# Kernel tuning notes

Hardware: AMD Instinct MI355X
Metric: run time of the kernel (lower is better)

The kernel has to match this reference:

```python
import jax, jax.numpy as jnp
import numpy as np

WIN = 7
SHIFT = 3
HEADS = 6
EPS = 1e-5


def _rel_pos_index(ws):
    coords = np.stack(np.meshgrid(np.arange(ws), np.arange(ws), indexing='ij')).reshape(2, -1)
    rel = (coords[:, :, None] - coords[:, None, :]).transpose(1, 2, 0)  # (N, N, 2)
    rel[..., 0] += ws - 1
    rel[..., 1] += ws - 1
    rel[..., 0] *= 2 * ws - 1
    return jnp.asarray(rel.sum(-1).reshape(-1))  # (N*N,)


def _attn_mask(H, W, ws, ss):
    img = np.zeros((H, W))
    sl = (slice(0, -ws), slice(-ws, -ss), slice(-ss, None))
    cnt = 0
    for hs in sl:
        for wss in sl:
            img[hs, wss] = cnt
            cnt += 1
    mw = img.reshape(H // ws, ws, W // ws, ws).transpose(0, 2, 1, 3).reshape(-1, ws * ws)
    am = mw[:, None, :] - mw[:, :, None]  # (nw, N, N): mw[j]-mw[i]
    return jnp.asarray(np.where(am != 0, -1e9, 0.0).astype(np.float32))


def _layernorm(x, g, b):
    mu = x.mean(-1, keepdims=True)
    var = ((x - mu) ** 2).mean(-1, keepdims=True)
    return (x - mu) * jax.lax.rsqrt(var + EPS) * g + b


def setup_inputs() -> dict:
    key = jax.random.key(0)
    ks = jax.random.split(key, 6)
    B, H, W, C = 4, 224, 224, 192
    return {
        'x': jax.random.normal(ks[0], (B, H * W, C), jnp.float32),
        'norm1_g': jnp.ones((C,), jnp.float32),
        'norm1_b': jnp.zeros((C,), jnp.float32),
        'qkv_w': jax.random.normal(ks[1], (C, 3 * C), jnp.float32) * 0.02,
        'qkv_b': jnp.zeros((3 * C,), jnp.float32),
        'rpb_table': jax.random.normal(ks[2], ((2 * WIN - 1) ** 2, HEADS), jnp.float32) * 0.02,
        'proj_w': jax.random.normal(ks[3], (C, C), jnp.float32) * 0.02,
        'proj_b': jnp.zeros((C,), jnp.float32),
        'norm2_g': jnp.ones((C,), jnp.float32),
        'norm2_b': jnp.zeros((C,), jnp.float32),
        'fc1_w': jax.random.normal(ks[4], (C, 4 * C), jnp.float32) * 0.02,
        'fc1_b': jnp.zeros((4 * C,), jnp.float32),
        'fc2_w': jax.random.normal(ks[5], (4 * C, C), jnp.float32) * 0.02,
        'fc2_b': jnp.zeros((C,), jnp.float32),
        'h': 224,
        'w': 224,
    }


def reference(x, norm1_g, norm1_b, qkv_w, qkv_b, rpb_table, proj_w, proj_b,
              norm2_g, norm2_b, fc1_w, fc1_b, fc2_w, fc2_b, h, w):
    B, L, C = x.shape
    ch = C // HEADS
    N = WIN * WIN
    nh, nw = h // WIN, w // WIN
    rel_idx = _rel_pos_index(WIN)
    mask = _attn_mask(h, w, WIN, SHIFT)  # (nh*nw, N, N)

    shortcut = x
    xn = _layernorm(x, norm1_g, norm1_b).reshape(B, h, w, C)
    xs = jnp.roll(xn, (-SHIFT, -SHIFT), axis=(1, 2))
    # window partition -> (B*nh*nw, N, C)
    xw = xs.reshape(B, nh, WIN, nw, WIN, C).transpose(0, 1, 3, 2, 4, 5).reshape(B * nh * nw, N, C)

    qkv = (xw @ qkv_w + qkv_b).reshape(-1, N, 3, HEADS, ch).transpose(2, 0, 3, 1, 4)
    q, k, v = qkv[0], qkv[1], qkv[2]  # (NW, HEADS, N, ch)
    scale = ch ** -0.5
    attn = jnp.einsum('whic,whjc->whij', q * scale, k)
    bias = rpb_table[rel_idx].reshape(N, N, HEADS).transpose(2, 0, 1)  # (HEADS, N, N)
    attn = attn + bias[None]
    attn = attn.reshape(B, nh * nw, HEADS, N, N) + mask[None, :, None]
    attn = jax.nn.softmax(attn, axis=-1).reshape(B * nh * nw, HEADS, N, N)

    out = jnp.einsum('whij,whjc->whic', attn, v).transpose(0, 2, 1, 3).reshape(-1, N, C)
    out = out @ proj_w + proj_b
    # window reverse + roll back
    out = out.reshape(B, nh, nw, WIN, WIN, C).transpose(0, 1, 3, 2, 4, 5).reshape(B, h, w, C)
    out = jnp.roll(out, (SHIFT, SHIFT), axis=(1, 2)).reshape(B, L, C)

    x = shortcut + out
    xn2 = _layernorm(x, norm2_g, norm2_b)
    hid = jax.nn.gelu(xn2 @ fc1_w + fc1_b, approximate=False)
    return x + (hid @ fc2_w + fc2_b)
```

## Files before the change

kernel.cpp:

```cpp
#include <hip/hip_runtime.h>
#include <stdint.h>

#define MB    50176
#define CDIM  192

typedef __attribute__((ext_vector_type(8))) short bf16x8;
typedef __attribute__((ext_vector_type(4))) float f32x4;

__device__ __forceinline__ float wsum(float v){
  #pragma unroll
  for (int m=32;m>=1;m>>=1) v += __shfl_xor(v,m,64);
  return v;
}
__device__ __forceinline__ float bfbits2f(uint32_t h){
  union{uint32_t u; float f;} x; x.u = h<<16; return x.f;
}
__device__ __forceinline__ uint16_t f2bfbits(float f){
  union{float ff; uint32_t u;} x; x.ff = f;
  return (uint16_t)((x.u + 0x7FFFu + ((x.u>>16)&1u)) >> 16);
}
__device__ __forceinline__ void gload16(const void* g, void* l){
  __builtin_amdgcn_global_load_lds(
      (const __attribute__((address_space(1))) uint32_t*)g,
      (__attribute__((address_space(3))) uint32_t*)l, 16, 0, 0);
}
__device__ __forceinline__ size_t row2tok(int r_g){
  int widx = r_g/49, tpos = r_g - widx*49;
  int b = widx>>10, rem = widx&1023;
  int h = (rem>>5)*7 + tpos/7 + 3; if (h>=224) h-=224;
  int w = (rem&31)*7 + (tpos - (tpos/7)*7) + 3; if (w>=224) w-=224;
  return (size_t)b*MB + (size_t)h*224 + w;
}

__global__ __launch_bounds__(256) void prep_kernel(
    const float* __restrict__ qkv_w, const float* __restrict__ proj_w,
    const float* __restrict__ fc1_w, const float* __restrict__ fc2_w,
    const float* __restrict__ rpb,
    uint16_t* __restrict__ qkvW, uint16_t* __restrict__ prjW,
    uint16_t* __restrict__ fc1W, uint16_t* __restrict__ fc2W,
    float* __restrict__ btbl){
  int idx = blockIdx.x*256 + threadIdx.x;
  if (idx < 110592){ int k=idx/576, n=idx-k*576; qkvW[n*192+k]=f2bfbits(qkv_w[idx]); return; }
  idx -= 110592;
  if (idx < 36864){ int k=idx/192, n=idx-k*192; prjW[n*192+k]=f2bfbits(proj_w[idx]); return; }
  idx -= 36864;
  if (idx < 147456){ int k=idx/768, n=idx-k*768; fc1W[n*192+k]=f2bfbits(fc1_w[idx]); return; }
  idx -= 147456;
  if (idx < 147456){ int k=idx/192, n=idx-k*192; fc2W[n*768+k]=f2bfbits(fc2_w[idx]); return; }
  idx -= 147456;
  if (idx >= 98304) return;
  int j = idx & 63, i = (idx>>6) & 63;
  int hd = (idx>>12) % 6, cls = (idx>>12)/6;
  float v = -1e9f;
  if (i < 49 && j < 49){
    int dh = i/7 - j/7, dw = i%7 - j%7;
    v = rpb[((dh+6)*13 + (dw+6))*6 + hd];
    int cH = cls>>1, cW = cls&1;
    int li = (cH ? (i/7 < 4 ? 1 : 2) : 0)*3 + (cW ? (i%7 < 4 ? 1 : 2) : 0);
    int lj = (cH ? (j/7 < 4 ? 1 : 2) : 0)*3 + (cW ? (j%7 < 4 ? 1 : 2) : 0);
    if (li != lj) v = -1e9f;
  }
  btbl[idx] = v;
}

__global__ __launch_bounds__(256) void ln1_kernel(
    const float* __restrict__ x, const float* __restrict__ g,
    const float* __restrict__ bt, uint16_t* __restrict__ dst, int row0){
  int wid_l = (int)((blockIdx.x*256u + threadIdx.x) >> 6);
  int lane  = threadIdx.x & 63;
  size_t sidx = row2tok(row0 + wid_l);
  const float* s = x + sidx*CDIM;
  float v0=s[lane], v1=s[lane+64], v2=s[lane+128];
  float mu  = wsum(v0+v1+v2) * (1.f/192.f);
  float var = wsum(v0*v0+v1*v1+v2*v2)*(1.f/192.f) - mu*mu;
  float rs  = rsqrtf(var + 1e-5f);
  uint16_t* d = dst + (size_t)wid_l*CDIM;
  d[lane]     = f2bfbits((v0-mu)*rs*g[lane]     + bt[lane]);
  d[lane+64]  = f2bfbits((v1-mu)*rs*g[lane+64]  + bt[lane+64]);
  d[lane+128] = f2bfbits((v2-mu)*rs*g[lane+128] + bt[lane+128]);
}

enum { EPI_QKV=0, EPI_FC1=2, EPI_FC2=3 };

template<int EPI, int K, int NN>
__global__ __launch_bounds__(256) void mgemm(
    const uint16_t* __restrict__ A, const uint16_t* __restrict__ WT,
    const float* __restrict__ bias, void* __restrict__ outp,
    const float* __restrict__ resid, int row0){
  __shared__ __attribute__((aligned(16))) char As[128*128];
  __shared__ __attribute__((aligned(16))) char Bs[64*128];
  const int tid  = threadIdx.x;
  const int lane = tid & 63;
  const int wid  = tid >> 6;
  const int brow = blockIdx.y * 128;
  const int bcol = blockIdx.x * 64;

  f32x4 acc[4][2];
  #pragma unroll
  for (int m=0;m<4;m++)
    #pragma unroll
    for (int n=0;n<2;n++) acc[m][n] = (f32x4){0.f,0.f,0.f,0.f};

  const int srow = lane >> 3;
  const int sg   = (lane & 7) ^ srow;
  const int wm = wid >> 1, wn = wid & 1;
  const int lrow16 = lane & 15, lkh = lane >> 4;

  for (int k0 = 0; k0 < K; k0 += 64){
    #pragma unroll
    for (int c = 0; c < 4; c++){
      int ch = wid*4 + c;
      gload16(A + (size_t)(brow + ch*8 + srow)*K + k0 + sg*8, As + ch*1024);
    }
    #pragma unroll
    for (int c = 0; c < 2; c++){
      int ch = wid*2 + c;
      gload16(WT + (size_t)(bcol + ch*8 + srow)*K + k0 + sg*8, Bs + ch*1024);
    }
    __syncthreads();

    bf16x8 af[4][2], bfr[2][2];
    #pragma unroll
    for (int m=0;m<4;m++)
      #pragma unroll
      for (int ks=0;ks<2;ks++){
        int arow = wm*64 + m*16 + lrow16;
        af[m][ks] = *(const bf16x8*)(As + arow*128 + (((ks*4+lkh) ^ (arow&7))<<4));
      }
    #pragma unroll
    for (int n=0;n<2;n++)
      #pragma unroll
      for (int ks=0;ks<2;ks++){
        int brn = wn*32 + n*16 + lrow16;
        bfr[n][ks] = *(const bf16x8*)(Bs + brn*128 + (((ks*4+lkh) ^ (brn&7))<<4));
      }
    #pragma unroll
    for (int m=0;m<4;m++)
      #pragma unroll
      for (int n=0;n<2;n++)
        #pragma unroll
        for (int ks=0;ks<2;ks++)
          acc[m][n] = __builtin_amdgcn_mfma_f32_16x16x32_bf16(
              af[m][ks], bfr[n][ks], acc[m][n], 0, 0, 0);
    __syncthreads();
  }

  float bi[2];
  #pragma unroll
  for (int n=0;n<2;n++) bi[n] = bias[bcol + wn*32 + n*16 + lrow16];
  #pragma unroll
  for (int m=0;m<4;m++){
    #pragma unroll
    for (int j=0;j<4;j++){
      int r = brow + wm*64 + m*16 + lkh*4 + j;
      if constexpr (EPI==EPI_QKV || EPI==EPI_FC1){
        #pragma unroll
        for (int n=0;n<2;n++){
          float v = acc[m][n][j] + bi[n];
          if constexpr (EPI==EPI_FC1)
            v = 0.5f*v*(1.f + erff(v*0.70710678118654752f));
          ((uint16_t*)outp)[(size_t)r*NN + bcol + wn*32 + n*16 + lrow16] = f2bfbits(v);
        }
      } else {
        size_t pr = row2tok(row0 + r)*CDIM;
        #pragma unroll
        for (int n=0;n<2;n++){
          size_t p = pr + bcol + wn*32 + n*16 + lrow16;
          ((float*)outp)[p] = acc[m][n][j] + bi[n] + resid[p];
        }
      }
    }
  }
}

__global__ __launch_bounds__(384) void proj_ln2(
    const uint16_t* __restrict__ A, const uint16_t* __restrict__ WT,
    const float* __restrict__ pbias, const float* __restrict__ x,
    const float* __restrict__ g2, const float* __restrict__ b2,
    float* __restrict__ xout, uint16_t* __restrict__ ln2out, int row0){
  __shared__ __attribute__((aligned(16))) char As[128*128];
  __shared__ __attribute__((aligned(16))) char Bs[192*128];
  __shared__ float stats[3][128][2];
  const int tid  = threadIdx.x;
  const int lane = tid & 63;
  const int wid  = tid >> 6;
  const int wm = wid >> 2, wn3 = wid & 3;
  const int pm = wid / 3, pn = wid - pm*3;
  const int brow = blockIdx.x * 128;
  const int srow = lane >> 3;
  const int sg   = (lane & 7) ^ srow;
  const int lrow16 = lane & 15, lkh = lane >> 4;
  (void)wm; (void)wn3;

  f32x4 acc[4][4];
  #pragma unroll
  for (int m=0;m<4;m++)
    #pragma unroll
    for (int n=0;n<4;n++) acc[m][n] = (f32x4){0.f,0.f,0.f,0.f};

  for (int k0 = 0; k0 < 192; k0 += 64){
    for (int ch = wid; ch < 16; ch += 6)
      gload16(A + (size_t)(brow + ch*8 + srow)*192 + k0 + sg*8, As + ch*1024);
    for (int ch = wid; ch < 24; ch += 6)
      gload16(WT + (size_t)(ch*8 + srow)*192 + k0 + sg*8, Bs + ch*1024);
    __syncthreads();

    bf16x8 af[4][2], bfr[4][2];
    #pragma unroll
    for (int m=0;m<4;m++)
      #pragma unroll
      for (int ks=0;ks<2;ks++){
        int arow = pm*64 + m*16 + lrow16;
        af[m][ks] = *(const bf16x8*)(As + arow*128 + (((ks*4+lkh) ^ (arow&7))<<4));
      }
    #pragma unroll
    for (int n=0;n<4;n++)
      #pragma unroll
      for (int ks=0;ks<2;ks++){
        int brn = pn*64 + n*16 + lrow16;
        bfr[n][ks] = *(const bf16x8*)(Bs + brn*128 + (((ks*4+lkh) ^ (brn&7))<<4));
      }
    #pragma unroll
    for (int m=0;m<4;m++)
      #pragma unroll
      for (int n=0;n<4;n++)
        #pragma unroll
        for (int ks=0;ks<2;ks++)
          acc[m][n] = __builtin_amdgcn_mfma_f32_16x16x32_bf16(
              af[m][ks], bfr[n][ks], acc[m][n], 0, 0, 0);
    __syncthreads();
  }

  float bi[4], g2v[4], b2v[4];
  #pragma unroll
  for (int n=0;n<4;n++){
    int c = pn*64 + n*16 + lrow16;
    bi[n] = pbias[c]; g2v[n] = g2[c]; b2v[n] = b2[c];
  }
  #pragma unroll
  for (int m=0;m<4;m++){
    #pragma unroll
    for (int j=0;j<4;j++){
      int r = pm*64 + m*16 + lkh*4 + j;
      size_t pr = row2tok(row0 + brow + r)*CDIM;
      float s1 = 0.f, s2 = 0.f;
      #pragma unroll
      for (int n=0;n<4;n++){
        int c = pn*64 + n*16 + lrow16;
        float y = acc[m][n][j] + bi[n] + x[pr + c];
        acc[m][n][j] = y;
        xout[pr + c] = y;
        s1 += y; s2 = fmaf(y, y, s2);
      }
      #pragma unroll
      for (int mk=1; mk<16; mk<<=1){
        s1 += __shfl_xor(s1, mk, 64);
        s2 += __shfl_xor(s2, mk, 64);
      }
      if (lrow16 == 0){ stats[pn][r][0] = s1; stats[pn][r][1] = s2; }
    }
  }
  __syncthreads();
  #pragma unroll
  for (int m=0;m<4;m++){
    #pragma unroll
    for (int j=0;j<4;j++){
      int r = pm*64 + m*16 + lkh*4 + j;
      float s1 = stats[0][r][0] + stats[1][r][0] + stats[2][r][0];
      float s2 = stats[0][r][1] + stats[1][r][1] + stats[2][r][1];
      float mu = s1*(1.f/192.f);
      float rs = rsqrtf(s2*(1.f/192.f) - mu*mu + 1e-5f);
      size_t pr = (size_t)(brow + r)*CDIM;
      #pragma unroll
      for (int n=0;n<4;n++){
        int c = pn*64 + n*16 + lrow16;
        ln2out[pr + c] = f2bfbits((acc[m][n][j]-mu)*rs*g2v[n] + b2v[n]);
      }
    }
  }
}

__global__ __launch_bounds__(64) void attn_kernel(
    const uint16_t* __restrict__ qkv, const float* __restrict__ btbl,
    uint16_t* __restrict__ attnout, int win0){
  const int bid  = blockIdx.x;
  const int widx = bid/6, hd = bid - widx*6;
  const int lane = threadIdx.x;
  const int r16 = lane & 15, t4 = lane >> 4;
  __shared__ uint16_t Vt[32][72];
  __shared__ uint16_t Pl[16][72];

  #pragma unroll
  for (int e=lane; e<32*16; e+=64){ Vt[e>>4][48 + (e&15)] = 0; }
  for (int ch = lane; ch < 196; ch += 64){
    int j = ch >> 2, c0 = (ch&3)*8;
    const uint16_t* src = qkv + ((size_t)widx*49 + j)*576 + hd*32 + 384 + c0;
    uint4 v = *(const uint4*)src;
    uint32_t u[4] = {v.x, v.y, v.z, v.w};
    #pragma unroll
    for (int q=0;q<8;q++) Vt[c0+q][j] = (uint16_t)(u[q>>1] >> ((q&1)*16));
  }

  bf16x8 kf[4], qf[4];
  #pragma unroll
  for (int jt=0;jt<4;jt++)
    kf[jt] = *(const bf16x8*)(qkv + ((size_t)widx*49 + jt*16 + r16)*576 + hd*32 + 192 + t4*8);
  #pragma unroll
  for (int it=0;it<4;it++)
    qf[it] = *(const bf16x8*)(qkv + ((size_t)widx*49 + it*16 + r16)*576 + hd*32 + t4*8);
  f32x4 acc[4][4];
  #pragma unroll
  for (int jt=0;jt<4;jt++)
    #pragma unroll
    for (int it=0;it<4;it++){
      acc[jt][it] = (f32x4){0.f,0.f,0.f,0.f};
      acc[jt][it] = __builtin_amdgcn_mfma_f32_16x16x32_bf16(kf[jt], qf[it], acc[jt][it], 0,0,0);
    }
  __syncthreads();

  const int gw = win0 + widx;
  const int cls = ((((gw&1023)>>5)==31)<<1) | ((gw&31)==31);
  const float* tb = btbl + ((size_t)(cls*6 + hd) << 12);
  const float scale = 0.17677669529663689f;

  bf16x8 bv[2][2];
  #pragma unroll
  for (int ct=0;ct<2;ct++)
    #pragma unroll
    for (int ks=0;ks<2;ks++)
      bv[ct][ks] = *(const bf16x8*)&Vt[ct*16 + r16][ks*32 + t4*8];

  #pragma unroll
  for (int it=0;it<4;it++){
    int i = it*16 + r16;
    float s[4][4];
    float m = -3.4e38f;
    #pragma unroll
    for (int jt=0;jt<4;jt++){
      float4 bvv = *(const float4*)(tb + i*64 + jt*16 + t4*4);
      float bb[4] = {bvv.x, bvv.y, bvv.z, bvv.w};
      #pragma unroll
      for (int r=0;r<4;r++){
        s[jt][r] = acc[jt][it][r]*scale + bb[r];
        m = fmaxf(m, s[jt][r]);
      }
    }
    m = fmaxf(m, __shfl_xor(m, 16, 64));
    m = fmaxf(m, __shfl_xor(m, 32, 64));
    float sum = 0.f;
    #pragma unroll
    for (int jt=0;jt<4;jt++)
      #pragma unroll
      for (int r=0;r<4;r++){
        s[jt][r] = __expf(s[jt][r] - m);
        sum += s[jt][r];
      }
    sum += __shfl_xor(sum, 16, 64);
    sum += __shfl_xor(sum, 32, 64);
    float inv = 1.f / sum;
    #pragma unroll
    for (int jt=0;jt<4;jt++){
      uint32_t lo = (uint32_t)f2bfbits(s[jt][0]*inv) | ((uint32_t)f2bfbits(s[jt][1]*inv) << 16);
      uint32_t hi = (uint32_t)f2bfbits(s[jt][2]*inv) | ((uint32_t)f2bfbits(s[jt][3]*inv) << 16);
      *(uint2*)&Pl[r16][jt*16 + t4*4] = make_uint2(lo, hi);
    }
    __syncthreads();

    f32x4 o[2];
    o[0] = (f32x4){0.f,0.f,0.f,0.f};
    o[1] = (f32x4){0.f,0.f,0.f,0.f};
    #pragma unroll
    for (int ks=0;ks<2;ks++){
      bf16x8 pa = *(const bf16x8*)&Pl[r16][ks*32 + t4*8];
      #pragma unroll
      for (int ct=0;ct<2;ct++)
        o[ct] = __builtin_amdgcn_mfma_f32_16x16x32_bf16(pa, bv[ct][ks], o[ct], 0,0,0);
    }
    #pragma unroll
    for (int r=0;r<4;r++){
      int i2 = it*16 + t4*4 + r;
      if (i2 < 49){
        size_t base = ((size_t)widx*49 + i2)*CDIM + hd*32;
        attnout[base + r16]      = f2bfbits(o[0][r]);
        attnout[base + 16 + r16] = f2bfbits(o[1][r]);
      }
    }
  }
}

extern "C" void kernel_launch(void* const* d_in, const int* in_sizes, int n_in,
                              void* d_out, int out_size, void* d_ws, size_t ws_size,
                              hipStream_t stream) {
  const float* x       = (const float*)d_in[0];
  const float* n1g     = (const float*)d_in[1];
  const float* n1b     = (const float*)d_in[2];
  const float* qkv_w   = (const float*)d_in[3];
  const float* qkv_b   = (const float*)d_in[4];
  const float* rpb     = (const float*)d_in[5];
  const float* proj_w  = (const float*)d_in[6];
  const float* proj_b  = (const float*)d_in[7];
  const float* n2g     = (const float*)d_in[8];
  const float* n2b     = (const float*)d_in[9];
  const float* fc1_w   = (const float*)d_in[10];
  const float* fc1_b   = (const float*)d_in[11];
  const float* fc2_w   = (const float*)d_in[12];
  const float* fc2_b   = (const float*)d_in[13];
  float* out = (float*)d_out;

  const size_t TBL = 221184 + 73728 + 294912 + 294912 + 393216;
  size_t need_full = (size_t)200704*CDIM*2 + (size_t)200704*768*2 + TBL;
  bool full = ws_size >= need_full;
  int T  = full ? 200704 : MB;
  int NC = full ? 1 : 4;
  int NW = T / 49;

  char* ws = (char*)d_ws;
  uint16_t* Abuf = (uint16_t*)ws;
  uint16_t* Bq   = (uint16_t*)(ws + (size_t)T*CDIM*2);
  char* wbase    = ws + (size_t)T*CDIM*2 + (size_t)T*768*2;
  uint16_t* qkvW = (uint16_t*)wbase;
  uint16_t* prjW = (uint16_t*)(wbase + 221184);
  uint16_t* fc1W = (uint16_t*)(wbase + 221184 + 73728);
  uint16_t* fc2W = (uint16_t*)(wbase + 221184 + 73728 + 294912);
  float*    btbl = (float*)(wbase + 221184 + 73728 + 294912 + 294912);

  prep_kernel<<<2112, 256, 0, stream>>>(qkv_w, proj_w, fc1_w, fc2_w, rpb,
                                        qkvW, prjW, fc1W, fc2W, btbl);

  for (int c = 0; c < NC; c++){
    int row0 = c*T, win0 = row0/49;
    ln1_kernel<<<T/4, 256, 0, stream>>>(x, n1g, n1b, Abuf, row0);
    mgemm<EPI_QKV, 192, 576>
        <<<dim3(9, T/128), 256, 0, stream>>>(Abuf, qkvW, qkv_b, (void*)Bq, nullptr, 0);
    attn_kernel<<<NW*6, 64, 0, stream>>>(Bq, btbl, Abuf, win0);
    proj_ln2<<<T/128, 384, 0, stream>>>(Abuf, prjW, proj_b, x, n2g, n2b,
                                        out, Abuf, row0);
    mgemm<EPI_FC1, 192, 768>
        <<<dim3(12, T/128), 256, 0, stream>>>(Abuf, fc1W, fc1_b, (void*)Bq, nullptr, 0);
    mgemm<EPI_FC2, 768, 192>
        <<<dim3(3, T/128), 256, 0, stream>>>(Bq, fc2W, fc2_b, (void*)out, out, row0);
  }
}
```

Baseline: 798.3 us.

## Fuse FC1+GELU and FC2 into one MLP kernel keeping hidden chunks in LDS

Replaces the separate FC1 (with GELU, writing a bf16 hidden tensor of width 768) and FC2 GEMM launches with a single kernel. Each 64-row block computes the hidden activations in chunks of 96, keeps them in shared memory and accumulates the FC2 output in registers, then adds bias and residual. This removes the global round trip of the large hidden tensor and lets the workspace shrink. In exchange, weights are read straight from global memory per block with no LDS staging, and fc1 weights are re-streamed for every 64-row block.

```diff
diff --git a/kernel.cpp b/kernel.cpp
--- a/kernel.cpp
+++ b/kernel.cpp
@@ -80,13 +80,9 @@
   d[lane+128] = f2bfbits((v2-mu)*rs*g[lane+128] + bt[lane+128]);
 }
 
-enum { EPI_QKV=0, EPI_FC1=2, EPI_FC2=3 };
-
-template<int EPI, int K, int NN>
-__global__ __launch_bounds__(256) void mgemm(
+__global__ __launch_bounds__(256) void qkv_gemm(
     const uint16_t* __restrict__ A, const uint16_t* __restrict__ WT,
-    const float* __restrict__ bias, void* __restrict__ outp,
-    const float* __restrict__ resid, int row0){
+    const float* __restrict__ bias, uint16_t* __restrict__ outp){
   __shared__ __attribute__((aligned(16))) char As[128*128];
   __shared__ __attribute__((aligned(16))) char Bs[64*128];
   const int tid  = threadIdx.x;
@@ -106,16 +102,16 @@
   const int wm = wid >> 1, wn = wid & 1;
   const int lrow16 = lane & 15, lkh = lane >> 4;
 
-  for (int k0 = 0; k0 < K; k0 += 64){
+  for (int k0 = 0; k0 < 192; k0 += 64){
     #pragma unroll
     for (int c = 0; c < 4; c++){
       int ch = wid*4 + c;
-      gload16(A + (size_t)(brow + ch*8 + srow)*K + k0 + sg*8, As + ch*1024);
+      gload16(A + (size_t)(brow + ch*8 + srow)*192 + k0 + sg*8, As + ch*1024);
     }
     #pragma unroll
     for (int c = 0; c < 2; c++){
       int ch = wid*2 + c;
-      gload16(WT + (size_t)(bcol + ch*8 + srow)*K + k0 + sg*8, Bs + ch*1024);
+      gload16(WT + (size_t)(bcol + ch*8 + srow)*192 + k0 + sg*8, Bs + ch*1024);
     }
     __syncthreads();
 
@@ -153,21 +149,10 @@
     #pragma unroll
     for (int j=0;j<4;j++){
       int r = brow + wm*64 + m*16 + lkh*4 + j;
-      if constexpr (EPI==EPI_QKV || EPI==EPI_FC1){
-        #pragma unroll
-        for (int n=0;n<2;n++){
-          float v = acc[m][n][j] + bi[n];
-          if constexpr (EPI==EPI_FC1)
-            v = 0.5f*v*(1.f + erff(v*0.70710678118654752f));
-          ((uint16_t*)outp)[(size_t)r*NN + bcol + wn*32 + n*16 + lrow16] = f2bfbits(v);
-        }
-      } else {
-        size_t pr = row2tok(row0 + r)*CDIM;
-        #pragma unroll
-        for (int n=0;n<2;n++){
-          size_t p = pr + bcol + wn*32 + n*16 + lrow16;
-          ((float*)outp)[p] = acc[m][n][j] + bi[n] + resid[p];
-        }
+      #pragma unroll
+      for (int n=0;n<2;n++){
+        float v = acc[m][n][j] + bi[n];
+        outp[(size_t)r*576 + bcol + wn*32 + n*16 + lrow16] = f2bfbits(v);
       }
     }
   }
@@ -184,13 +169,11 @@
   const int tid  = threadIdx.x;
   const int lane = tid & 63;
   const int wid  = tid >> 6;
-  const int wm = wid >> 2, wn3 = wid & 3;
   const int pm = wid / 3, pn = wid - pm*3;
   const int brow = blockIdx.x * 128;
   const int srow = lane >> 3;
   const int sg   = (lane & 7) ^ srow;
   const int lrow16 = lane & 15, lkh = lane >> 4;
-  (void)wm; (void)wn3;
 
   f32x4 acc[4][4];
   #pragma unroll
@@ -275,6 +258,101 @@
       for (int n=0;n<4;n++){
         int c = pn*64 + n*16 + lrow16;
         ln2out[pr + c] = f2bfbits((acc[m][n][j]-mu)*rs*g2v[n] + b2v[n]);
+      }
+    }
+  }
+}
+
+__global__ __launch_bounds__(384) void mlp_kernel(
+    const uint16_t* __restrict__ A,
+    const uint16_t* __restrict__ W1T,
+    const uint16_t* __restrict__ W2T,
+    const float* __restrict__ b1, const float* __restrict__ b2,
+    const float* __restrict__ resid,
+    float* __restrict__ out, int row0){
+  __shared__ uint16_t hidc[64][104];
+  const int tid  = threadIdx.x;
+  const int lane = tid & 63, wid = tid >> 6;
+  const int pm = wid / 3, pn = wid - pm*3;
+  const int r16 = lane & 15, t4 = lane >> 4;
+  const int brow = blockIdx.x * 64;
+
+  bf16x8 af[2][6];
+  #pragma unroll
+  for (int m=0;m<2;m++)
+    #pragma unroll
+    for (int ks=0;ks<6;ks++)
+      af[m][ks] = *(const bf16x8*)(A + (size_t)(brow + pm*32 + m*16 + r16)*192 + ks*32 + t4*8);
+
+  f32x4 aco[2][4];
+  #pragma unroll
+  for (int m=0;m<2;m++)
+    #pragma unroll
+    for (int n=0;n<4;n++) aco[m][n] = (f32x4){0.f,0.f,0.f,0.f};
+
+  for (int hc=0; hc<8; hc++){
+    f32x4 ach[2][2];
+    #pragma unroll
+    for (int m=0;m<2;m++)
+      #pragma unroll
+      for (int n=0;n<2;n++) ach[m][n] = (f32x4){0.f,0.f,0.f,0.f};
+    #pragma unroll
+    for (int ks=0;ks<6;ks++){
+      bf16x8 bw[2];
+      #pragma unroll
+      for (int n=0;n<2;n++)
+        bw[n] = *(const bf16x8*)(W1T + (size_t)(hc*96 + pn*32 + n*16 + r16)*192 + ks*32 + t4*8);
+      #pragma unroll
+      for (int m=0;m<2;m++)
+        #pragma unroll
+        for (int n=0;n<2;n++)
+          ach[m][n] = __builtin_amdgcn_mfma_f32_16x16x32_bf16(af[m][ks], bw[n], ach[m][n], 0,0,0);
+    }
+    #pragma unroll
+    for (int m=0;m<2;m++)
+      #pragma unroll
+      for (int n=0;n<2;n++){
+        float bb = b1[hc*96 + pn*32 + n*16 + r16];
+        #pragma unroll
+        for (int j=0;j<4;j++){
+          int rl = pm*32 + m*16 + t4*4 + j;
+          int c  = pn*32 + n*16 + r16;
+          float v = ach[m][n][j] + bb;
+          v = 0.5f*v*(1.f + erff(v*0.70710678118654752f));
+          hidc[rl][c] = f2bfbits(v);
+        }
+      }
+    __syncthreads();
+    #pragma unroll
+    for (int ks=0;ks<3;ks++){
+      bf16x8 pa[2];
+      #pragma unroll
+      for (int m=0;m<2;m++)
+        pa[m] = *(const bf16x8*)&hidc[pm*32 + m*16 + r16][ks*32 + t4*8];
+      #pragma unroll
+      for (int n=0;n<4;n++){
+        bf16x8 bw = *(const bf16x8*)(W2T + (size_t)(pn*64 + n*16 + r16)*768 + hc*96 + ks*32 + t4*8);
+        #pragma unroll
+        for (int m=0;m<2;m++)
+          aco[m][n] = __builtin_amdgcn_mfma_f32_16x16x32_bf16(pa[m], bw, aco[m][n], 0,0,0);
+      }
+    }
+    __syncthreads();
+  }
+
+  float b2v[4];
+  #pragma unroll
+  for (int n=0;n<4;n++) b2v[n] = b2[pn*64 + n*16 + r16];
+  #pragma unroll
+  for (int m=0;m<2;m++){
+    #pragma unroll
+    for (int j=0;j<4;j++){
+      int r = brow + pm*32 + m*16 + t4*4 + j;
+      size_t pr = row2tok(row0 + r)*CDIM;
+      #pragma unroll
+      for (int n=0;n<4;n++){
+        int c = pn*64 + n*16 + r16;
+        out[pr + c] = aco[m][n][j] + b2v[n] + resid[pr + c];
       }
     }
   }
@@ -408,7 +486,7 @@
   float* out = (float*)d_out;
 
   const size_t TBL = 221184 + 73728 + 294912 + 294912 + 393216;
-  size_t need_full = (size_t)200704*CDIM*2 + (size_t)200704*768*2 + TBL;
+  size_t need_full = (size_t)200704*CDIM*2 + (size_t)200704*576*2 + TBL;
   bool full = ws_size >= need_full;
   int T  = full ? 200704 : MB;
   int NC = full ? 1 : 4;
@@ -417,7 +495,7 @@
   char* ws = (char*)d_ws;
   uint16_t* Abuf = (uint16_t*)ws;
   uint16_t* Bq   = (uint16_t*)(ws + (size_t)T*CDIM*2);
-  char* wbase    = ws + (size_t)T*CDIM*2 + (size_t)T*768*2;
+  char* wbase    = ws + (size_t)T*CDIM*2 + (size_t)T*576*2;
   uint16_t* qkvW = (uint16_t*)wbase;
   uint16_t* prjW = (uint16_t*)(wbase + 221184);
   uint16_t* fc1W = (uint16_t*)(wbase + 221184 + 73728);
@@ -430,14 +508,11 @@
   for (int c = 0; c < NC; c++){
     int row0 = c*T, win0 = row0/49;
     ln1_kernel<<<T/4, 256, 0, stream>>>(x, n1g, n1b, Abuf, row0);
-    mgemm<EPI_QKV, 192, 576>
-        <<<dim3(9, T/128), 256, 0, stream>>>(Abuf, qkvW, qkv_b, (void*)Bq, nullptr, 0);
+    qkv_gemm<<<dim3(9, T/128), 256, 0, stream>>>(Abuf, qkvW, qkv_b, Bq);
     attn_kernel<<<NW*6, 64, 0, stream>>>(Bq, btbl, Abuf, win0);
     proj_ln2<<<T/128, 384, 0, stream>>>(Abuf, prjW, proj_b, x, n2g, n2b,
                                         out, Abuf, row0);
-    mgemm<EPI_FC1, 192, 768>
-        <<<dim3(12, T/128), 256, 0, stream>>>(Abuf, fc1W, fc1_b, (void*)Bq, nullptr, 0);
-    mgemm<EPI_FC2, 768, 192>
-        <<<dim3(3, T/128), 256, 0, stream>>>(Bq, fc2W, fc2_b, (void*)out, out, row0);
-  }
-}
+    mlp_kernel<<<T/64, 384, 0, stream>>>(Abuf, fc1W, fc2W, fc1_b, fc2_b,
+                                         out, out, row0);
+  }
+}
```

After: 994.7 us. +24.6%, slower.

## Widen GEMM tiles to 128x192 with 6 waves and pack 4 attention heads per block

Applied to the files above, without the earlier changes.

The generic GEMM moves from a 128x64 tile with 4 waves to a 128x192 tile with 6 waves, so each A tile is loaded once per 192 output columns instead of once per 64. This cuts redundant global loads of the activation matrix, at the cost of more LDS, more registers per wave and fewer blocks (the FC2 GEMM now has a single column block). The attention kernel now runs four independent window-head pairs per 256-thread block, each wave with its own LDS slices. Block barriers are replaced by lgkmcnt waits, and the QK^T product is computed per 16-row slice to lower register pressure.

```diff
diff --git a/kernel.cpp b/kernel.cpp
--- a/kernel.cpp
+++ b/kernel.cpp
@@ -6,6 +6,8 @@
 
 typedef __attribute__((ext_vector_type(8))) short bf16x8;
 typedef __attribute__((ext_vector_type(4))) float f32x4;
+
+#define WFENCE asm volatile("s_waitcnt lgkmcnt(0)" ::: "memory")
 
 __device__ __forceinline__ float wsum(float v){
   #pragma unroll
@@ -83,61 +85,58 @@
 enum { EPI_QKV=0, EPI_FC1=2, EPI_FC2=3 };
 
 template<int EPI, int K, int NN>
-__global__ __launch_bounds__(256) void mgemm(
+__global__ __launch_bounds__(384) void mgemm(
     const uint16_t* __restrict__ A, const uint16_t* __restrict__ WT,
     const float* __restrict__ bias, void* __restrict__ outp,
     const float* __restrict__ resid, int row0){
   __shared__ __attribute__((aligned(16))) char As[128*128];
-  __shared__ __attribute__((aligned(16))) char Bs[64*128];
+  __shared__ __attribute__((aligned(16))) char Bs[192*128];
   const int tid  = threadIdx.x;
   const int lane = tid & 63;
   const int wid  = tid >> 6;
+  const int pm = wid / 3, pn = wid - pm*3;
   const int brow = blockIdx.y * 128;
-  const int bcol = blockIdx.x * 64;
-
-  f32x4 acc[4][2];
-  #pragma unroll
-  for (int m=0;m<4;m++)
-    #pragma unroll
-    for (int n=0;n<2;n++) acc[m][n] = (f32x4){0.f,0.f,0.f,0.f};
-
+  const int cbase = blockIdx.x * 192;
   const int srow = lane >> 3;
   const int sg   = (lane & 7) ^ srow;
-  const int wm = wid >> 1, wn = wid & 1;
-  const int lrow16 = lane & 15, lkh = lane >> 4;
+  const int r16 = lane & 15, t4 = lane >> 4;
+
+  f32x4 acc[4][4];
+  #pragma unroll
+  for (int m=0;m<4;m++)
+    #pragma unroll
+    for (int n=0;n<4;n++) acc[m][n] = (f32x4){0.f,0.f,0.f,0.f};
 
   for (int k0 = 0; k0 < K; k0 += 64){
-    #pragma unroll
-    for (int c = 0; c < 4; c++){
-      int ch = wid*4 + c;
-      gload16(A + (size_t)(brow + ch*8 + srow)*K + k0 + sg*8, As + ch*1024);
-    }
-    #pragma unroll
-    for (int c = 0; c < 2; c++){
-      int ch = wid*2 + c;
-      gload16(WT + (size_t)(bcol + ch*8 + srow)*K + k0 + sg*8, Bs + ch*1024);
+    for (int ch = wid; ch < 40; ch += 6){
+      if (ch < 16)
+        gload16(A + (size_t)(brow + ch*8 + srow)*K + k0 + sg*8, As + ch*1024);
+      else {
+        int bc = ch - 16;
+        gload16(WT + (size_t)(cbase + bc*8 + srow)*K + k0 + sg*8, Bs + bc*1024);
+      }
     }
     __syncthreads();
 
-    bf16x8 af[4][2], bfr[2][2];
+    bf16x8 af[4][2], bfr[4][2];
     #pragma unroll
     for (int m=0;m<4;m++)
       #pragma unroll
       for (int ks=0;ks<2;ks++){
-        int arow = wm*64 + m*16 + lrow16;
-        af[m][ks] = *(const bf16x8*)(As + arow*128 + (((ks*4+lkh) ^ (arow&7))<<4));
-      }
-    #pragma unroll
-    for (int n=0;n<2;n++)
+        int arow = pm*64 + m*16 + r16;
+        af[m][ks] = *(const bf16x8*)(As + arow*128 + (((ks*4+t4) ^ (arow&7))<<4));
+      }
+    #pragma unroll
+    for (int n=0;n<4;n++)
       #pragma unroll
       for (int ks=0;ks<2;ks++){
-        int brn = wn*32 + n*16 + lrow16;
-        bfr[n][ks] = *(const bf16x8*)(Bs + brn*128 + (((ks*4+lkh) ^ (brn&7))<<4));
+        int brn = pn*64 + n*16 + r16;
+        bfr[n][ks] = *(const bf16x8*)(Bs + brn*128 + (((ks*4+t4) ^ (brn&7))<<4));
       }
     #pragma unroll
     for (int m=0;m<4;m++)
       #pragma unroll
-      for (int n=0;n<2;n++)
+      for (int n=0;n<4;n++)
         #pragma unroll
         for (int ks=0;ks<2;ks++)
           acc[m][n] = __builtin_amdgcn_mfma_f32_16x16x32_bf16(
@@ -145,27 +144,27 @@
     __syncthreads();
   }
 
-  float bi[2];
-  #pragma unroll
-  for (int n=0;n<2;n++) bi[n] = bias[bcol + wn*32 + n*16 + lrow16];
+  float bi[4];
+  #pragma unroll
+  for (int n=0;n<4;n++) bi[n] = bias[cbase + pn*64 + n*16 + r16];
   #pragma unroll
   for (int m=0;m<4;m++){
     #pragma unroll
     for (int j=0;j<4;j++){
-      int r = brow + wm*64 + m*16 + lkh*4 + j;
+      int r = brow + pm*64 + m*16 + t4*4 + j;
       if constexpr (EPI==EPI_QKV || EPI==EPI_FC1){
         #pragma unroll
-        for (int n=0;n<2;n++){
+        for (int n=0;n<4;n++){
           float v = acc[m][n][j] + bi[n];
           if constexpr (EPI==EPI_FC1)
             v = 0.5f*v*(1.f + erff(v*0.70710678118654752f));
-          ((uint16_t*)outp)[(size_t)r*NN + bcol + wn*32 + n*16 + lrow16] = f2bfbits(v);
+          ((uint16_t*)outp)[(size_t)r*NN + cbase + pn*64 + n*16 + r16] = f2bfbits(v);
         }
       } else {
         size_t pr = row2tok(row0 + r)*CDIM;
         #pragma unroll
-        for (int n=0;n<2;n++){
-          size_t p = pr + bcol + wn*32 + n*16 + lrow16;
+        for (int n=0;n<4;n++){
+          size_t p = pr + cbase + pn*64 + n*16 + r16;
           ((float*)outp)[p] = acc[m][n][j] + bi[n] + resid[p];
         }
       }
@@ -184,13 +183,11 @@
   const int tid  = threadIdx.x;
   const int lane = tid & 63;
   const int wid  = tid >> 6;
-  const int wm = wid >> 2, wn3 = wid & 3;
   const int pm = wid / 3, pn = wid - pm*3;
   const int brow = blockIdx.x * 128;
   const int srow = lane >> 3;
   const int sg   = (lane & 7) ^ srow;
   const int lrow16 = lane & 15, lkh = lane >> 4;
-  (void)wm; (void)wn3;
 
   f32x4 acc[4][4];
   #pragma unroll
@@ -280,58 +277,55 @@
   }
 }
 
-__global__ __launch_bounds__(64) void attn_kernel(
+__global__ __launch_bounds__(256) void attn_kernel(
     const uint16_t* __restrict__ qkv, const float* __restrict__ btbl,
     uint16_t* __restrict__ attnout, int win0){
-  const int bid  = blockIdx.x;
-  const int widx = bid/6, hd = bid - widx*6;
-  const int lane = threadIdx.x;
+  const int wv   = threadIdx.x >> 6;
+  const int lane = threadIdx.x & 63;
+  const int whd  = blockIdx.x*4 + wv;
+  const int widx = whd/6, hd = whd - widx*6;
   const int r16 = lane & 15, t4 = lane >> 4;
-  __shared__ uint16_t Vt[32][72];
-  __shared__ uint16_t Pl[16][72];
-
-  #pragma unroll
-  for (int e=lane; e<32*16; e+=64){ Vt[e>>4][48 + (e&15)] = 0; }
+  __shared__ uint16_t Vt[4][32][72];
+  __shared__ uint16_t Pl[4][16][72];
+
+  #pragma unroll
+  for (int e=lane; e<32*16; e+=64){ Vt[wv][e>>4][48 + (e&15)] = 0; }
   for (int ch = lane; ch < 196; ch += 64){
     int j = ch >> 2, c0 = (ch&3)*8;
     const uint16_t* src = qkv + ((size_t)widx*49 + j)*576 + hd*32 + 384 + c0;
     uint4 v = *(const uint4*)src;
     uint32_t u[4] = {v.x, v.y, v.z, v.w};
     #pragma unroll
-    for (int q=0;q<8;q++) Vt[c0+q][j] = (uint16_t)(u[q>>1] >> ((q&1)*16));
-  }
-
-  bf16x8 kf[4], qf[4];
+    for (int q=0;q<8;q++) Vt[wv][c0+q][j] = (uint16_t)(u[q>>1] >> ((q&1)*16));
+  }
+
+  bf16x8 kf[4];
   #pragma unroll
   for (int jt=0;jt<4;jt++)
     kf[jt] = *(const bf16x8*)(qkv + ((size_t)widx*49 + jt*16 + r16)*576 + hd*32 + 192 + t4*8);
-  #pragma unroll
-  for (int it=0;it<4;it++)
-    qf[it] = *(const bf16x8*)(qkv + ((size_t)widx*49 + it*16 + r16)*576 + hd*32 + t4*8);
-  f32x4 acc[4][4];
-  #pragma unroll
-  for (int jt=0;jt<4;jt++)
-    #pragma unroll
-    for (int it=0;it<4;it++){
-      acc[jt][it] = (f32x4){0.f,0.f,0.f,0.f};
-      acc[jt][it] = __builtin_amdgcn_mfma_f32_16x16x32_bf16(kf[jt], qf[it], acc[jt][it], 0,0,0);
-    }
-  __syncthreads();
 
   const int gw = win0 + widx;
   const int cls = ((((gw&1023)>>5)==31)<<1) | ((gw&31)==31);
   const float* tb = btbl + ((size_t)(cls*6 + hd) << 12);
   const float scale = 0.17677669529663689f;
 
+  WFENCE;
   bf16x8 bv[2][2];
   #pragma unroll
   for (int ct=0;ct<2;ct++)
     #pragma unroll
     for (int ks=0;ks<2;ks++)
-      bv[ct][ks] = *(const bf16x8*)&Vt[ct*16 + r16][ks*32 + t4*8];
-
-  #pragma unroll
-  for (int it=0;it<4;it++){
+      bv[ct][ks] = *(const bf16x8*)&Vt[wv][ct*16 + r16][ks*32 + t4*8];
+
+  #pragma unroll 1
+  for (int it=0; it<4; it++){
+    bf16x8 qf = *(const bf16x8*)(qkv + ((size_t)widx*49 + it*16 + r16)*576 + hd*32 + t4*8);
+    f32x4 acc[4];
+    #pragma unroll
+    for (int jt=0;jt<4;jt++){
+      acc[jt] = (f32x4){0.f,0.f,0.f,0.f};
+      acc[jt] = __builtin_amdgcn_mfma_f32_16x16x32_bf16(kf[jt], qf, acc[jt], 0,0,0);
+    }
     int i = it*16 + r16;
     float s[4][4];
     float m = -3.4e38f;
@@ -341,7 +335,7 @@
       float bb[4] = {bvv.x, bvv.y, bvv.z, bvv.w};
       #pragma unroll
       for (int r=0;r<4;r++){
-        s[jt][r] = acc[jt][it][r]*scale + bb[r];
+        s[jt][r] = acc[jt][r]*scale + bb[r];
         m = fmaxf(m, s[jt][r]);
       }
     }
@@ -362,16 +356,16 @@
     for (int jt=0;jt<4;jt++){
       uint32_t lo = (uint32_t)f2bfbits(s[jt][0]*inv) | ((uint32_t)f2bfbits(s[jt][1]*inv) << 16);
       uint32_t hi = (uint32_t)f2bfbits(s[jt][2]*inv) | ((uint32_t)f2bfbits(s[jt][3]*inv) << 16);
-      *(uint2*)&Pl[r16][jt*16 + t4*4] = make_uint2(lo, hi);
-    }
-    __syncthreads();
+      *(uint2*)&Pl[wv][r16][jt*16 + t4*4] = make_uint2(lo, hi);
+    }
+    WFENCE;
 
     f32x4 o[2];
     o[0] = (f32x4){0.f,0.f,0.f,0.f};
     o[1] = (f32x4){0.f,0.f,0.f,0.f};
     #pragma unroll
     for (int ks=0;ks<2;ks++){
-      bf16x8 pa = *(const bf16x8*)&Pl[r16][ks*32 + t4*8];
+      bf16x8 pa = *(const bf16x8*)&Pl[wv][r16][ks*32 + t4*8];
       #pragma unroll
       for (int ct=0;ct<2;ct++)
         o[ct] = __builtin_amdgcn_mfma_f32_16x16x32_bf16(pa, bv[ct][ks], o[ct], 0,0,0);
@@ -431,13 +425,13 @@
     int row0 = c*T, win0 = row0/49;
     ln1_kernel<<<T/4, 256, 0, stream>>>(x, n1g, n1b, Abuf, row0);
     mgemm<EPI_QKV, 192, 576>
-        <<<dim3(9, T/128), 256, 0, stream>>>(Abuf, qkvW, qkv_b, (void*)Bq, nullptr, 0);
-    attn_kernel<<<NW*6, 64, 0, stream>>>(Bq, btbl, Abuf, win0);
+        <<<dim3(3, T/128), 384, 0, stream>>>(Abuf, qkvW, qkv_b, (void*)Bq, nullptr, 0);
+    attn_kernel<<<NW*6/4, 256, 0, stream>>>(Bq, btbl, Abuf, win0);
     proj_ln2<<<T/128, 384, 0, stream>>>(Abuf, prjW, proj_b, x, n2g, n2b,
                                         out, Abuf, row0);
     mgemm<EPI_FC1, 192, 768>
-        <<<dim3(12, T/128), 256, 0, stream>>>(Abuf, fc1W, fc1_b, (void*)Bq, nullptr, 0);
+        <<<dim3(4, T/128), 384, 0, stream>>>(Abuf, fc1W, fc1_b, (void*)Bq, nullptr, 0);
     mgemm<EPI_FC2, 768, 192>
-        <<<dim3(3, T/128), 256, 0, stream>>>(Bq, fc2W, fc2_b, (void*)out, out, row0);
-  }
-}
+        <<<dim3(1, T/128), 384, 0, stream>>>(Bq, fc2W, fc2_b, (void*)out, out, row0);
+  }
+}
```

Result: slower. 852.4 us (+6.8%).
